# Optimization experiments

Measured on AMD Instinct MI355X. Metric: run time of the kernel, lower is better.

Reference implementation:

```python
import jax, jax.numpy as jnp
import numpy as np

INPUT_DIM = 1024
HIDDEN_DIM = 2048
NUM_EMB = 4096
EMB_DIM = 256
N = 65536


def setup_inputs() -> dict:
    key = jax.random.key(0)
    ks = jax.random.split(key, 10)
    s = lambda fan_in: 1.0 / np.sqrt(fan_in)
    return {
        "x": jax.random.normal(ks[0], (N, INPUT_DIM), dtype=jnp.float32),
        # encoder: Linear(input_dim, hidden) -> ReLU -> Linear(hidden, emb)
        "W1": jax.random.uniform(ks[1], (INPUT_DIM, HIDDEN_DIM), jnp.float32, -s(INPUT_DIM), s(INPUT_DIM)),
        "b1": jax.random.uniform(ks[2], (HIDDEN_DIM,), jnp.float32, -s(INPUT_DIM), s(INPUT_DIM)),
        "W2": jax.random.uniform(ks[3], (HIDDEN_DIM, EMB_DIM), jnp.float32, -s(HIDDEN_DIM), s(HIDDEN_DIM)),
        "b2": jax.random.uniform(ks[4], (EMB_DIM,), jnp.float32, -s(HIDDEN_DIM), s(HIDDEN_DIM)),
        # codebook (nn.Embedding weight)
        "codebook": jax.random.normal(ks[5], (NUM_EMB, EMB_DIM), dtype=jnp.float32),
        # decoder: Linear(emb, hidden) -> ReLU -> Linear(hidden, input_dim)
        "W3": jax.random.uniform(ks[6], (EMB_DIM, HIDDEN_DIM), jnp.float32, -s(EMB_DIM), s(EMB_DIM)),
        "b3": jax.random.uniform(ks[7], (HIDDEN_DIM,), jnp.float32, -s(EMB_DIM), s(EMB_DIM)),
        "W4": jax.random.uniform(ks[8], (HIDDEN_DIM, INPUT_DIM), jnp.float32, -s(HIDDEN_DIM), s(HIDDEN_DIM)),
        "b4": jax.random.uniform(ks[9], (INPUT_DIM,), jnp.float32, -s(HIDDEN_DIM), s(HIDDEN_DIM)),
    }


def reference(x, W1, b1, W2, b2, codebook, W3, b3, W4, b4):
    # encoder
    h = jax.nn.relu(x @ W1 + b1)
    encoded = h @ W2 + b2                      # [N, E]
    # cdist (squared form; argmin is identical to Euclidean argmin)
    enc_sq = jnp.sum(encoded * encoded, axis=-1, keepdims=True)   # [N, 1]
    cb_sq = jnp.sum(codebook * codebook, axis=-1)                 # [K]
    d2 = enc_sq - 2.0 * (encoded @ codebook.T) + cb_sq            # [N, K]
    indices = jnp.argmin(d2, axis=-1)                             # [N]
    quantized = codebook[indices]                                 # [N, E]
    # decoder
    h2 = jax.nn.relu(quantized @ W3 + b3)
    decoded = h2 @ W4 + b4
    return (quantized, decoded)
```

## Files before the change

kernel.cpp:

```cpp
#include <hip/hip_runtime.h>

#define N_ROWS 65536
#define IN_DIM 1024
#define HID    2048
#define EMB    256
#define NCODE  4096

typedef __attribute__((ext_vector_type(8))) short bf16x8;
typedef __attribute__((ext_vector_type(4))) float f32x4;

__device__ __forceinline__ unsigned short f2bf(float v) {
    unsigned u = __float_as_uint(v);
    u += 0x7FFFu + ((u >> 16) & 1u);
    return (unsigned short)(u >> 16);
}
__device__ __forceinline__ float bf2f(unsigned short h) {
    return __uint_as_float(((unsigned)h) << 16);
}
__device__ __forceinline__ void gload16(const unsigned short* g, unsigned short* l) {
    __builtin_amdgcn_global_load_lds(
        (const __attribute__((address_space(1))) unsigned int*)g,
        (__attribute__((address_space(3))) unsigned int*)l, 16, 0, 0);
}

template<int SPLIT>
__global__ __launch_bounds__(256) void k_conv_w(
    const float* __restrict__ src, unsigned short* __restrict__ dh,
    unsigned short* __restrict__ dl, int NC, int nkt)
{
    const int t = threadIdx.x;
    const int nt = blockIdx.x, kt = blockIdx.y;
    const int kk = t >> 2, j4 = (t & 3) << 2;
    const int k0 = kt << 6, n0 = nt << 4;
    float4 v = *(const float4*)(src + (size_t)(k0 + kk) * NC + n0 + j4);
    size_t tb = ((size_t)nt * nkt + kt) * 1024 + ((kk >> 3) * 128) + (kk & 7);
    float vv[4] = {v.x, v.y, v.z, v.w};
    #pragma unroll
    for (int j = 0; j < 4; ++j) {
        unsigned short h = f2bf(vv[j]);
        dh[tb + (size_t)(j4 + j) * 8] = h;
        if (SPLIT) dl[tb + (size_t)(j4 + j) * 8] = f2bf(vv[j] - bf2f(h));
    }
}

__global__ __launch_bounds__(256) void k_conv_a(
    const float* __restrict__ src, unsigned short* __restrict__ dst, int Kw, int nkt)
{
    const int t = threadIdx.x;
    const int mt = blockIdx.x, kt = blockIdx.y;
    const int rr = t >> 4, k4 = (t & 15) << 2;
    float4 v = *(const float4*)(src + (size_t)(mt * 16 + rr) * Kw + kt * 64 + k4);
    size_t addr = ((size_t)mt * nkt + kt) * 1024 + (k4 >> 3) * 128 + rr * 8 + (k4 & 7);
    ushort4 h = { f2bf(v.x), f2bf(v.y), f2bf(v.z), f2bf(v.w) };
    *(ushort4*)&dst[addr] = h;
}

__global__ __launch_bounds__(256) void k_conv_a2(
    const float* __restrict__ src, unsigned short* __restrict__ dh,
    unsigned short* __restrict__ dl, int Kw, int nkt)
{
    const int t = threadIdx.x;
    const int mt = blockIdx.x, kt = blockIdx.y;
    const int rr = t >> 4, k4 = (t & 15) << 2;
    float4 v = *(const float4*)(src + (size_t)(mt * 16 + rr) * Kw + kt * 64 + k4);
    size_t addr = ((size_t)mt * nkt + kt) * 1024 + (k4 >> 3) * 128 + rr * 8 + (k4 & 7);
    ushort4 h = { f2bf(v.x), f2bf(v.y), f2bf(v.z), f2bf(v.w) };
    ushort4 lo = { f2bf(v.x - bf2f(h.x)), f2bf(v.y - bf2f(h.y)),
                   f2bf(v.z - bf2f(h.z)), f2bf(v.w - bf2f(h.w)) };
    *(ushort4*)&dh[addr] = h;
    *(ushort4*)&dl[addr] = lo;
}

__global__ __launch_bounds__(256) void k_conv_cb(
    const float* __restrict__ cb, unsigned short* __restrict__ ch,
    unsigned short* __restrict__ cl_, float* __restrict__ halfsq)
{
    const int t = threadIdx.x;
    const int ct = blockIdx.x;
    const int cl = t >> 4, f = t & 15;
    const int code = (ct << 4) + cl;
    float ssq = 0.f;
    #pragma unroll
    for (int it = 0; it < 4; ++it) {
        const int k4 = (f << 2) + (it << 6);
        float4 v = *(const float4*)(cb + (size_t)code * EMB + k4);
        ssq += v.x * v.x + v.y * v.y + v.z * v.z + v.w * v.w;
        size_t tb = ((size_t)(ct * 4 + (k4 >> 6))) * 1024 + ((k4 >> 3) & 7) * 128 + cl * 8 + (k4 & 7);
        ushort4 h = { f2bf(v.x), f2bf(v.y), f2bf(v.z), f2bf(v.w) };
        *(ushort4*)&ch[tb] = h;
        ushort4 lo = { f2bf(v.x - bf2f(h.x)), f2bf(v.y - bf2f(h.y)),
                       f2bf(v.z - bf2f(h.z)), f2bf(v.w - bf2f(h.w)) };
        *(ushort4*)&cl_[tb] = lo;
    }
    #pragma unroll
    for (int off = 1; off <= 8; off <<= 1) ssq += __shfl_xor(ssq, off);
    if (f == 0) halfsq[code] = 0.5f * ssq;
}

template<int SPLIT, int AFMT, int OUTT>
__global__ __launch_bounds__(512, 1) void k_layer2(
    const float* __restrict__ A, const unsigned short* __restrict__ At,
    const unsigned short* __restrict__ Atl, int a_nkt,
    int lda, int K,
    const unsigned short* __restrict__ Bh, const unsigned short* __restrict__ Bl,
    int b_nkt, const float* __restrict__ bias, int biasoff,
    float* __restrict__ out, unsigned short* __restrict__ outt,
    unsigned short* __restrict__ outt2,
    int outw, int relu, int init, int ny_log2)
{
    constexpr int BUFSZ = SPLIT ? 32768 : 24576;
    constexpr int AL = 8192;
    constexpr int BH = SPLIT ? 16384 : 8192;
    __shared__ __align__(16) unsigned short s_mem[2 * BUFSZ];

    const int t = threadIdx.x;
    const int id = blockIdx.x;
    const int m_low = id & 7, rest = id >> 3;
    const int nb = rest & ((1 << ny_log2) - 1);
    const int m0 = (((rest >> ny_log2) << 3) | m_low) * 128;
    const int nb0 = nb * 256;
    const int lane = t & 63, wv = t >> 6;
    const int wm = wv >> 2, wn = wv & 3;
    const int g = lane >> 4, rr = lane & 15;
    const int nt = K >> 6;

    f32x4 acc[4][4];
    #pragma unroll
    for (int mi = 0; mi < 4; ++mi)
        #pragma unroll
        for (int ni = 0; ni < 4; ++ni) acc[mi][ni] = (f32x4){0.f, 0.f, 0.f, 0.f};

    #define STAGE_DMA(buf, ktile)                                                      \
        {                                                                              \
            unsigned short* base_ = &s_mem[(buf) * BUFSZ];                             \
            _Pragma("unroll")                                                          \
            for (int jj = 0; jj < 2; ++jj) {                                           \
                const int j_ = wv * 2 + jj;                                            \
                const size_t gt_ = ((size_t)(nb0 / 16 + j_) * b_nkt + (ktile)) * 1024; \
                _Pragma("unroll")                                                      \
                for (int hf = 0; hf < 2; ++hf)                                         \
                    gload16(Bh + gt_ + hf * 512 + lane * 8,                            \
                            base_ + BH + j_ * 1024 + hf * 512);                        \
            }                                                                          \
            if (AFMT >= 1) {                                                           \
                const size_t ga_ = ((size_t)(m0 / 16 + wv) * a_nkt + (ktile)) * 1024;  \
                _Pragma("unroll")                                                      \
                for (int hf = 0; hf < 2; ++hf)                                         \
                    gload16(At + ga_ + hf * 512 + lane * 8,                            \
                            base_ + wv * 1024 + hf * 512);                             \
                if (AFMT == 2) {                                                       \
                    _Pragma("unroll")                                                  \
                    for (int hf = 0; hf < 2; ++hf)                                     \
                        gload16(Atl + ga_ + hf * 512 + lane * 8,                       \
                                base_ + AL + wv * 1024 + hf * 512);                    \
                }                                                                      \
            }                                                                          \
        }

    #define A_LOAD(ktile, pv)                                                          \
        {                                                                              \
            _Pragma("unroll")                                                          \
            for (int it = 0; it < 4; ++it) {                                           \
                int f_ = t + (it << 9);                                                \
                int r_ = f_ >> 4, k4_ = (f_ & 15) << 2;                                \
                pv[it] = *(const float4*)(A + (size_t)(m0 + r_) * lda + (ktile) * 64 + k4_); \
            }                                                                          \
        }

    #define A_WRITE(buf, pv)                                                           \
        {                                                                              \
            unsigned short* base_ = &s_mem[(buf) * BUFSZ];                             \
            _Pragma("unroll")                                                          \
            for (int it = 0; it < 4; ++it) {                                           \
                int f_ = t + (it << 9);                                                \
                int r_ = f_ >> 4, k4_ = (f_ & 15) << 2;                                \
                int mt_ = r_ >> 4, rl_ = r_ & 15, kb_ = k4_ >> 3, e_ = k4_ & 7;        \
                int addr_ = mt_ * 1024 + kb_ * 128 + ((rl_ ^ kb_) << 3) + e_;          \
                float4 v_ = pv[it];                                                    \
                ushort4 hi_, lo_;                                                      \
                hi_.x = f2bf(v_.x); hi_.y = f2bf(v_.y); hi_.z = f2bf(v_.z); hi_.w = f2bf(v_.w); \
                *(ushort4*)&base_[addr_] = hi_;                                        \
                if (SPLIT) {                                                           \
                    lo_.x = f2bf(v_.x - bf2f(hi_.x)); lo_.y = f2bf(v_.y - bf2f(hi_.y)); \
                    lo_.z = f2bf(v_.z - bf2f(hi_.z)); lo_.w = f2bf(v_.w - bf2f(hi_.w)); \
                    *(ushort4*)&base_[AL + addr_] = lo_;                               \
                }                                                                      \
            }                                                                          \
        }

    #define COMPUTE(buf, ktile)                                                        \
        {                                                                              \
            const unsigned short* base_ = &s_mem[(buf) * BUFSZ];                       \
            __builtin_amdgcn_s_setprio(1);                                             \
            _Pragma("unroll")                                                          \
            for (int s = 0; s < 2; ++s) {                                              \
                const int kb = (s << 2) + g;                                           \
                bf16x8 a_h[4], a_l[4], b_h[4], b_l[4];                                 \
                _Pragma("unroll")                                                      \
                for (int i = 0; i < 4; ++i) {                                          \
                    int arow = (AFMT == 0) ? (((rr ^ kb) & 15) << 3) : (rr << 3);      \
                    int aaddr = (wm * 4 + i) * 1024 + kb * 128 + arow;                 \
                    a_h[i] = *(const bf16x8*)&base_[aaddr];                            \
                    if (SPLIT) a_l[i] = *(const bf16x8*)&base_[AL + aaddr];            \
                    int baddr = (wn * 4 + i) * 1024 + kb * 128 + (rr << 3);            \
                    b_h[i] = *(const bf16x8*)&base_[BH + baddr];                       \
                    if (SPLIT)                                                         \
                        b_l[i] = *(const bf16x8*)(Bl +                                 \
                            ((size_t)(nb0 / 16 + wn * 4 + i) * b_nkt + (ktile)) * 1024 \
                            + kb * 128 + (rr << 3));                                   \
                }                                                                      \
                _Pragma("unroll")                                                      \
                for (int mi = 0; mi < 4; ++mi)                                         \
                    _Pragma("unroll")                                                  \
                    for (int ni = 0; ni < 4; ++ni) {                                   \
                        acc[mi][ni] = __builtin_amdgcn_mfma_f32_16x16x32_bf16(a_h[mi], b_h[ni], acc[mi][ni], 0, 0, 0); \
                        if (SPLIT) {                                                   \
                            acc[mi][ni] = __builtin_amdgcn_mfma_f32_16x16x32_bf16(a_l[mi], b_h[ni], acc[mi][ni], 0, 0, 0); \
                            acc[mi][ni] = __builtin_amdgcn_mfma_f32_16x16x32_bf16(a_h[mi], b_l[ni], acc[mi][ni], 0, 0, 0); \
                        }                                                              \
                    }                                                                  \
            }                                                                          \
            __builtin_amdgcn_s_setprio(0);                                             \
        }

    float4 pv[4];
    STAGE_DMA(0, 0)
    if (AFMT == 0) {
        A_LOAD(0, pv)
        A_WRITE(0, pv)
    }
    asm volatile("s_waitcnt vmcnt(0) lgkmcnt(0)" ::: "memory");
    __builtin_amdgcn_s_barrier();
    __builtin_amdgcn_sched_barrier(0);

    int cur = 0;
    for (int kt = 0; kt < nt; ++kt) {
        if (kt + 1 < nt) {
            STAGE_DMA(cur ^ 1, kt + 1)
            if (AFMT == 0) A_LOAD(kt + 1, pv)
        }
        COMPUTE(cur, kt)
        if (AFMT == 0) { if (kt + 1 < nt) A_WRITE(cur ^ 1, pv) }
        asm volatile("s_waitcnt vmcnt(0) lgkmcnt(0)" ::: "memory");
        __builtin_amdgcn_s_barrier();
        __builtin_amdgcn_sched_barrier(0);
        cur ^= 1;
    }
    #undef STAGE_DMA
    #undef A_LOAD
    #undef A_WRITE
    #undef COMPUTE

    if (OUTT == 0) {
        float* sf = (float*)s_mem;
        for (int rm = 0; rm < 2; ++rm) {
            if (wm == rm) {
                #pragma unroll
                for (int mi = 0; mi < 4; ++mi)
                    #pragma unroll
                    for (int ni = 0; ni < 4; ++ni)
                        #pragma unroll
                        for (int rg = 0; rg < 4; ++rg)
                            sf[(mi * 16 + g * 4 + rg) * 256 + wn * 64 + ni * 16 + rr] = acc[mi][ni][rg];
            }
            __syncthreads();
            #pragma unroll
            for (int it = 0; it < 8; ++it) {
                int f = t + (it << 9);
                int r = f >> 6, c4 = (f & 63) << 2;
                float4 v = *(const float4*)&sf[r * 256 + c4];
                int gr = m0 + rm * 64 + r, gc = nb0 + c4;
                float* op = out + (size_t)gr * outw + gc;
                if (init) {
                    v.x += bias[biasoff + gc + 0]; v.y += bias[biasoff + gc + 1];
                    v.z += bias[biasoff + gc + 2]; v.w += bias[biasoff + gc + 3];
                } else {
                    float4 o = *(const float4*)op;
                    v.x += o.x; v.y += o.y; v.z += o.z; v.w += o.w;
                }
                if (relu) {
                    v.x = fmaxf(v.x, 0.f); v.y = fmaxf(v.y, 0.f);
                    v.z = fmaxf(v.z, 0.f); v.w = fmaxf(v.w, 0.f);
                }
                *(float4*)op = v;
            }
            __syncthreads();
        }
    } else {
        const int npass = (OUTT == 2) ? 2 : 1;
        for (int pass = 0; pass < npass; ++pass) {
            #pragma unroll
            for (int mi = 0; mi < 4; ++mi)
                #pragma unroll
                for (int ni = 0; ni < 4; ++ni) {
                    const int c = wn * 64 + ni * 16 + rr;
                    float bb = bias[biasoff + nb0 + c];
                    #pragma unroll
                    for (int rg = 0; rg < 4; ++rg) {
                        float v = acc[mi][ni][rg] + bb;
                        if (relu) v = fmaxf(v, 0.f);
                        unsigned short hi = f2bf(v);
                        unsigned short w = (pass == 0) ? hi : f2bf(v - bf2f(hi));
                        int addr = ((wm * 4 + mi) * 4 + wn) * 1024
                                 + (ni * 2 + (rr >> 3)) * 128 + (g * 4 + rg) * 8 + (rr & 7);
                        s_mem[addr] = w;
                    }
                }
            __syncthreads();
            unsigned short* dst = (pass == 0) ? outt : outt2;
            #pragma unroll
            for (int it = 0; it < 8; ++it) {
                int f = t + (it << 9);
                int tl = f >> 7, w8 = f & 127;
                size_t gaddr = ((size_t)(m0 / 16 + (tl >> 2)) * outw + nb0 / 64 + (tl & 3)) * 1024;
                *(float4*)(dst + gaddr + w8 * 8) = *(const float4*)&s_mem[tl * 1024 + w8 * 8];
            }
            __syncthreads();
        }
    }
}

__global__ __launch_bounds__(512, 2) void k_dist(
    float* encq, const unsigned short* __restrict__ ch,
    const unsigned short* __restrict__ cl,
    const float* __restrict__ hsq, const float* __restrict__ cb)
{
    __shared__ __align__(16) unsigned short s_cb[2][16384];
    __shared__ int s_c1[256], s_c2[256];

    const int t = threadIdx.x;
    const int lane = t & 63, wv = t >> 6;
    const int g = lane >> 4, rr = lane & 15;
    const int r0 = blockIdx.x * 256;

    bf16x8 eh[2][8], el[2][8];
    #pragma unroll
    for (int rg = 0; rg < 2; ++rg) {
        const float* ep = encq + (size_t)(r0 + wv * 32 + rg * 16 + rr) * EMB + g * 8;
        #pragma unroll
        for (int s = 0; s < 8; ++s) {
            float4 v0 = *(const float4*)(ep + s * 32);
            float4 v1 = *(const float4*)(ep + s * 32 + 4);
            float vv[8] = {v0.x, v0.y, v0.z, v0.w, v1.x, v1.y, v1.z, v1.w};
            bf16x8 a, b;
            #pragma unroll
            for (int j = 0; j < 8; ++j) {
                unsigned short h = f2bf(vv[j]);
                a[j] = (short)h;
                b[j] = (short)f2bf(vv[j] - bf2f(h));
            }
            eh[rg][s] = a; el[rg][s] = b;
        }
    }
    float b1v[2][4], b2v[2][4]; int i1v[2][4], i2v[2][4];
    #pragma unroll
    for (int rg = 0; rg < 2; ++rg)
        #pragma unroll
        for (int r2 = 0; r2 < 4; ++r2) {
            b1v[rg][r2] = -1e30f; b2v[rg][r2] = -1e30f;
            i1v[rg][r2] = 0; i2v[rg][r2] = 0;
        }

    #define STAGE(buf, c)                                                              \
        {                                                                              \
            const unsigned short* gh_ = ch + (size_t)(c) * 8192 + wv * 1024;           \
            const unsigned short* gl_ = cl + (size_t)(c) * 8192 + wv * 1024;           \
            _Pragma("unroll")                                                          \
            for (int i_ = 0; i_ < 2; ++i_) {                                           \
                gload16(gh_ + i_ * 512 + lane * 8, &s_cb[buf][wv * 1024 + i_ * 512]);  \
                gload16(gl_ + i_ * 512 + lane * 8, &s_cb[buf][8192 + wv * 1024 + i_ * 512]); \
            }                                                                          \
        }

    #define COMPUTE(cur, c, hv_)                                                       \
        {                                                                              \
            f32x4 ahh[2][2], ahl[2][2], alh[2][2];                                     \
            _Pragma("unroll")                                                          \
            for (int rg = 0; rg < 2; ++rg)                                             \
                _Pragma("unroll")                                                      \
                for (int ci = 0; ci < 2; ++ci) {                                       \
                    ahh[rg][ci] = (f32x4){0.f, 0.f, 0.f, 0.f};                         \
                    ahl[rg][ci] = (f32x4){0.f, 0.f, 0.f, 0.f};                         \
                    alh[rg][ci] = (f32x4){0.f, 0.f, 0.f, 0.f};                         \
                }                                                                      \
            __builtin_amdgcn_s_setprio(1);                                             \
            _Pragma("unroll")                                                          \
            for (int s = 0; s < 8; ++s) {                                              \
                const int ktile = s >> 1, kb = ((s & 1) << 2) + g;                     \
                _Pragma("unroll")                                                      \
                for (int ci = 0; ci < 2; ++ci) {                                       \
                    const int off = (ci * 4 + ktile) * 1024 + kb * 128 + rr * 8;       \
                    bf16x8 bh = *(const bf16x8*)&s_cb[cur][off];                       \
                    bf16x8 bl = *(const bf16x8*)&s_cb[cur][8192 + off];                \
                    _Pragma("unroll")                                                  \
                    for (int rg = 0; rg < 2; ++rg) {                                   \
                        ahh[rg][ci] = __builtin_amdgcn_mfma_f32_16x16x32_bf16(eh[rg][s], bh, ahh[rg][ci], 0, 0, 0); \
                        ahl[rg][ci] = __builtin_amdgcn_mfma_f32_16x16x32_bf16(eh[rg][s], bl, ahl[rg][ci], 0, 0, 0); \
                        alh[rg][ci] = __builtin_amdgcn_mfma_f32_16x16x32_bf16(el[rg][s], bh, alh[rg][ci], 0, 0, 0); \
                    }                                                                  \
                }                                                                      \
            }                                                                          \
            __builtin_amdgcn_s_setprio(0);                                             \
            _Pragma("unroll")                                                          \
            for (int rg = 0; rg < 2; ++rg)                                             \
                _Pragma("unroll")                                                      \
                for (int ci = 0; ci < 2; ++ci) {                                       \
                    f32x4 av = ahh[rg][ci] + ahl[rg][ci] + alh[rg][ci];                \
                    const int code = ((c) << 5) + (ci << 4) + rr;                      \
                    const float hs = __shfl(hv_, ci * 16 + rr);                        \
                    _Pragma("unroll")                                                  \
                    for (int r2 = 0; r2 < 4; ++r2) {                                   \
                        float v = av[r2] - hs;                                         \
                        bool bt1 = (v > b1v[rg][r2]) || (v == b1v[rg][r2] && code < i1v[rg][r2]); \
                        bool bt2 = (v > b2v[rg][r2]) || (v == b2v[rg][r2] && code < i2v[rg][r2]); \
                        if (bt1) { b2v[rg][r2] = b1v[rg][r2]; i2v[rg][r2] = i1v[rg][r2]; \
                                   b1v[rg][r2] = v; i1v[rg][r2] = code; }              \
                        else if (bt2) { b2v[rg][r2] = v; i2v[rg][r2] = code; }         \
                    }                                                                  \
                }                                                                      \
        }

    STAGE(0, 0)
    int cur = 0;
    for (int c = 0; c < 127; ++c) {
        STAGE(cur ^ 1, c + 1)
        float hv_ = hsq[(c << 5) + (lane & 31)];
        asm volatile("s_waitcnt vmcnt(5)" ::: "memory");
        __builtin_amdgcn_s_barrier();
        __builtin_amdgcn_sched_barrier(0);
        COMPUTE(cur, c, hv_)
        asm volatile("" ::: "memory");
        __builtin_amdgcn_s_barrier();
        cur ^= 1;
    }
    {
        float hv_ = hsq[(127 << 5) + (lane & 31)];
        asm volatile("s_waitcnt vmcnt(0)" ::: "memory");
        __builtin_amdgcn_s_barrier();
        __builtin_amdgcn_sched_barrier(0);
        COMPUTE(cur, 127, hv_)
    }
    #undef STAGE
    #undef COMPUTE

    #pragma unroll
    for (int off = 1; off <= 8; off <<= 1) {
        #pragma unroll
        for (int rg = 0; rg < 2; ++rg)
            #pragma unroll
            for (int r2 = 0; r2 < 4; ++r2) {
                float ob1 = __shfl_xor(b1v[rg][r2], off), ob2 = __shfl_xor(b2v[rg][r2], off);
                int oi1 = __shfl_xor(i1v[rg][r2], off), oi2 = __shfl_xor(i2v[rg][r2], off);
                bool ofirst = (ob1 > b1v[rg][r2]) || (ob1 == b1v[rg][r2] && oi1 < i1v[rg][r2]);
                if (ofirst) {
                    bool mysec = (b1v[rg][r2] > ob2) || (b1v[rg][r2] == ob2 && i1v[rg][r2] < oi2);
                    b2v[rg][r2] = mysec ? b1v[rg][r2] : ob2; i2v[rg][r2] = mysec ? i1v[rg][r2] : oi2;
                    b1v[rg][r2] = ob1; i1v[rg][r2] = oi1;
                } else {
                    bool osec = (ob1 > b2v[rg][r2]) || (ob1 == b2v[rg][r2] && oi1 < i2v[rg][r2]);
                    b2v[rg][r2] = osec ? ob1 : b2v[rg][r2]; i2v[rg][r2] = osec ? oi1 : i2v[rg][r2];
                }
            }
    }
    if (rr == 0) {
        #pragma unroll
        for (int rg = 0; rg < 2; ++rg)
            #pragma unroll
            for (int r2 = 0; r2 < 4; ++r2) {
                int rl = wv * 32 + rg * 16 + g * 4 + r2;
                s_c1[rl] = i1v[rg][r2]; s_c2[rl] = i2v[rg][r2];
            }
    }
    __syncthreads();

    for (int rloc = 0; rloc < 32; ++rloc) {
        const int row = wv * 32 + rloc;
        const int c1 = s_c1[row], c2 = s_c2[row];
        float4 ev = *(const float4*)(encq + (size_t)(r0 + row) * EMB + lane * 4);
        float4 v1 = *(const float4*)(cb + (size_t)c1 * EMB + lane * 4);
        float4 v2 = *(const float4*)(cb + (size_t)c2 * EMB + lane * 4);
        float d1 = ev.x * v1.x + ev.y * v1.y + ev.z * v1.z + ev.w * v1.w;
        float d2 = ev.x * v2.x + ev.y * v2.y + ev.z * v2.z + ev.w * v2.w;
        #pragma unroll
        for (int off = 1; off <= 32; off <<= 1) {
            d1 += __shfl_xor(d1, off);
            d2 += __shfl_xor(d2, off);
        }
        if (lane == 0) {
            float s1 = d1 - hsq[c1], s2 = d2 - hsq[c2];
            bool keep1 = (s1 > s2) || (s1 == s2 && c1 < c2);
            s_c1[row] = keep1 ? c1 : c2;
        }
    }
    __syncthreads();
    #pragma unroll
    for (int it = 0; it < 32; ++it) {
        int f = t + (it << 9);
        int row = f >> 6, c4 = (f & 63) << 2;
        int bi = s_c1[row];
        *(float4*)(encq + (size_t)(r0 + row) * EMB + c4) =
            *(const float4*)(cb + (size_t)bi * EMB + c4);
    }
}

__global__ __launch_bounds__(256) void k_dec_fb(
    const float* __restrict__ qz,
    const float* __restrict__ W3, const float* __restrict__ b3,
    const float* __restrict__ W4, const float* __restrict__ b4,
    float* __restrict__ outd) {
    __shared__ float s_q[8][EMB];
    __shared__ float s_h2[8][HID];
    const int t = threadIdx.x;
    const int row0 = blockIdx.x * 8;
    #pragma unroll
    for (int r = 0; r < 8; ++r) s_q[r][t] = qz[(size_t)(row0 + r) * EMB + t];
    __syncthreads();
    for (int gg = 0; gg < 8; ++gg) {
        const int j = (gg << 8) + t;
        float acc[8];
        #pragma unroll
        for (int r = 0; r < 8; ++r) acc[r] = 0.f;
        const float* wp = W3 + j;
        for (int e = 0; e < EMB; e += 4) {
            const float w0 = wp[(size_t)(e + 0) * HID];
            const float w1v = wp[(size_t)(e + 1) * HID];
            const float w2v = wp[(size_t)(e + 2) * HID];
            const float w3v = wp[(size_t)(e + 3) * HID];
            #pragma unroll
            for (int r = 0; r < 8; ++r) {
                const float4 qv = *reinterpret_cast<const float4*>(&s_q[r][e]);
                acc[r] = fmaf(qv.x, w0, acc[r]);
                acc[r] = fmaf(qv.y, w1v, acc[r]);
                acc[r] = fmaf(qv.z, w2v, acc[r]);
                acc[r] = fmaf(qv.w, w3v, acc[r]);
            }
        }
        const float bb = b3[j];
        #pragma unroll
        for (int r = 0; r < 8; ++r) s_h2[r][j] = fmaxf(acc[r] + bb, 0.f);
    }
    __syncthreads();
    float acc4[8][4];
    #pragma unroll
    for (int r = 0; r < 8; ++r)
        #pragma unroll
        for (int ci = 0; ci < 4; ++ci) acc4[r][ci] = 0.f;
    const float* w4p = W4 + t;
    for (int k = 0; k < HID; k += 4) {
        float wv[4][4];
        #pragma unroll
        for (int ki = 0; ki < 4; ++ki)
            #pragma unroll
            for (int ci = 0; ci < 4; ++ci)
                wv[ki][ci] = w4p[(size_t)(k + ki) * IN_DIM + (ci << 8)];
        #pragma unroll
        for (int r = 0; r < 8; ++r) {
            const float4 hv = *reinterpret_cast<const float4*>(&s_h2[r][k]);
            #pragma unroll
            for (int ci = 0; ci < 4; ++ci) {
                acc4[r][ci] = fmaf(hv.x, wv[0][ci], acc4[r][ci]);
                acc4[r][ci] = fmaf(hv.y, wv[1][ci], acc4[r][ci]);
                acc4[r][ci] = fmaf(hv.z, wv[2][ci], acc4[r][ci]);
                acc4[r][ci] = fmaf(hv.w, wv[3][ci], acc4[r][ci]);
            }
        }
    }
    #pragma unroll
    for (int ci = 0; ci < 4; ++ci) {
        const float bb = b4[(ci << 8) + t];
        #pragma unroll
        for (int r = 0; r < 8; ++r)
            outd[(size_t)(row0 + r) * IN_DIM + (ci << 8) + t] = acc4[r][ci] + bb;
    }
}

extern "C" void kernel_launch(void* const* d_in, const int* in_sizes, int n_in,
                              void* d_out, int out_size, void* d_ws, size_t ws_size,
                              hipStream_t stream) {
    const float* x  = (const float*)d_in[0];
    const float* W1 = (const float*)d_in[1];
    const float* b1 = (const float*)d_in[2];
    const float* W2 = (const float*)d_in[3];
    const float* b2 = (const float*)d_in[4];
    const float* cb = (const float*)d_in[5];
    const float* W3 = (const float*)d_in[6];
    const float* b3 = (const float*)d_in[7];
    const float* W4 = (const float*)d_in[8];
    const float* b4 = (const float*)d_in[9];

    float* outq = (float*)d_out;
    float* outd = outq + (size_t)N_ROWS * EMB;

    unsigned short* ou = (unsigned short*)outd;
    unsigned short* W1Th = ou;
    unsigned short* W1Tl = ou + 2097152;
    unsigned short* W2Th = ou + 4194304;
    unsigned short* W2Tl = ou + 4718592;
    unsigned short* cbh  = ou + 5242880;
    unsigned short* cbl  = ou + 6291456;
    float* halfsq = outd + 3670016;
    unsigned short* h_hi = (unsigned short*)(outd + 4194304);
    unsigned short* h_lo = h_hi + 33554432;
    unsigned short* qt = (unsigned short*)(outd + 58720256);
    float* enc = outq;

    const bool fastdec = ws_size >= (size_t)72351744;
    unsigned short* W3Th = (unsigned short*)d_ws;
    unsigned short* W4Th = W3Th + 524288;
    unsigned short* h2t  = (unsigned short*)((char*)d_ws + 5242880);
    unsigned short* xt_hi = h2t;
    unsigned short* xt_lo = h2t + 16777216;

    k_conv_w<1><<<dim3(128, 16), 256, 0, stream>>>(W1, W1Th, W1Tl, HID, 16);
    k_conv_w<1><<<dim3(16, 32), 256, 0, stream>>>(W2, W2Th, W2Tl, EMB, 32);
    k_conv_cb<<<256, 256, 0, stream>>>(cb, cbh, cbl, halfsq);
    if (fastdec) {
        k_conv_w<0><<<dim3(128, 4), 256, 0, stream>>>(W3, W3Th, nullptr, HID, 4);
        k_conv_w<0><<<dim3(64, 32), 256, 0, stream>>>(W4, W4Th, nullptr, IN_DIM, 32);
    }
    if (fastdec) {
        for (int s = 0; s < 4; ++s) {
            k_conv_a2<<<dim3(1024, 16), 256, 0, stream>>>(
                x + (size_t)s * 16777216, xt_hi, xt_lo, IN_DIM, 16);
            k_layer2<1, 2, 2><<<1024, 512, 0, stream>>>(
                nullptr, xt_hi, xt_lo, 16, 0, IN_DIM,
                W1Th, W1Tl, 16, b1, 0,
                nullptr, h_hi, h_lo, 32, 1, 0, 3);
            k_layer2<1, 2, 0><<<128, 512, 0, stream>>>(
                nullptr, h_hi, h_lo, 32, 0, HID,
                W2Th, W2Tl, 32, b2, 0,
                enc + (size_t)s * 4194304, nullptr, nullptr, EMB, 0, 1, 0);
        }
    } else {
        for (int q = 0; q < 4; ++q) {
            k_layer2<1, 0, 2><<<1024, 512, 0, stream>>>(
                x, nullptr, nullptr, 0, IN_DIM, IN_DIM,
                W1Th + (size_t)q * 524288, W1Tl + (size_t)q * 524288, 16,
                b1, q * 512, nullptr, h_hi, h_lo, 8, 1, 0, 1);
            k_layer2<1, 2, 0><<<512, 512, 0, stream>>>(
                nullptr, h_hi, h_lo, 8, 0, 512,
                W2Th + (size_t)q * 8192, W2Tl + (size_t)q * 8192, 32,
                b2, 0, enc, nullptr, nullptr, EMB, 0, q == 0, 0);
        }
    }
    k_dist<<<256, 512, 0, stream>>>(enc, cbh, cbl, halfsq, cb);
    if (fastdec) {
        k_conv_a<<<dim3(4096, 4), 256, 0, stream>>>(outq, qt, EMB, 4);
        for (int s = 0; s < 4; ++s) {
            const size_t roff = (size_t)s * 16384;
            k_layer2<0, 1, 1><<<1024, 512, 0, stream>>>(
                nullptr, qt + (size_t)s * 4194304, nullptr, 4, 0, EMB,
                W3Th, nullptr, 4,
                b3, 0, nullptr, h2t, nullptr, 32, 1, 0, 3);
            k_layer2<0, 1, 0><<<512, 512, 0, stream>>>(
                nullptr, h2t, nullptr, 32, 0, HID,
                W4Th, nullptr, 32,
                b4, 0, outd + roff * IN_DIM, nullptr, nullptr, IN_DIM, 0, 1, 2);
        }
    } else {
        k_dec_fb<<<N_ROWS / 8, 256, 0, stream>>>(outq, W3, b3, W4, b4, outd);
    }
}
```

Measured before the change: 2.359 ms.

## Restructure GEMM k-loop waits for DMA paths and fuse quantized bf16 conversion

For the DMA-fed A formats, the GEMM k-loop now issues the next stage's loads and waits only on the previous stage's outstanding loads with a partial vmcnt, then computes. A second barrier follows the compute, replacing the full vmcnt(0)/lgkmcnt(0) drain after compute, so prefetch overlaps compute. Separately, k_dist now writes the bf16 tiled copy of the quantized rows directly, removing the separate k_conv_a launch and its re-read of the quantized output. The hard-coded vmcnt counts depend on how many loads STAGE_DMA issues per format and could race if that count differs.

```diff
diff --git a/kernel.cpp b/kernel.cpp
--- a/kernel.cpp
+++ b/kernel.cpp
@@ -41,18 +41,6 @@
         dh[tb + (size_t)(j4 + j) * 8] = h;
         if (SPLIT) dl[tb + (size_t)(j4 + j) * 8] = f2bf(vv[j] - bf2f(h));
     }
-}
-
-__global__ __launch_bounds__(256) void k_conv_a(
-    const float* __restrict__ src, unsigned short* __restrict__ dst, int Kw, int nkt)
-{
-    const int t = threadIdx.x;
-    const int mt = blockIdx.x, kt = blockIdx.y;
-    const int rr = t >> 4, k4 = (t & 15) << 2;
-    float4 v = *(const float4*)(src + (size_t)(mt * 16 + rr) * Kw + kt * 64 + k4);
-    size_t addr = ((size_t)mt * nkt + kt) * 1024 + (k4 >> 3) * 128 + rr * 8 + (k4 & 7);
-    ushort4 h = { f2bf(v.x), f2bf(v.y), f2bf(v.z), f2bf(v.w) };
-    *(ushort4*)&dst[addr] = h;
 }
 
 __global__ __launch_bounds__(256) void k_conv_a2(
@@ -235,15 +223,30 @@
 
     int cur = 0;
     for (int kt = 0; kt < nt; ++kt) {
-        if (kt + 1 < nt) {
-            STAGE_DMA(cur ^ 1, kt + 1)
-            if (AFMT == 0) A_LOAD(kt + 1, pv)
-        }
-        COMPUTE(cur, kt)
-        if (AFMT == 0) { if (kt + 1 < nt) A_WRITE(cur ^ 1, pv) }
-        asm volatile("s_waitcnt vmcnt(0) lgkmcnt(0)" ::: "memory");
-        __builtin_amdgcn_s_barrier();
-        __builtin_amdgcn_sched_barrier(0);
+        if (AFMT >= 1) {
+            if (kt + 1 < nt) {
+                STAGE_DMA(cur ^ 1, kt + 1)
+                if (AFMT == 2) asm volatile("s_waitcnt vmcnt(8)" ::: "memory");
+                else           asm volatile("s_waitcnt vmcnt(6)" ::: "memory");
+            } else {
+                asm volatile("s_waitcnt vmcnt(0)" ::: "memory");
+            }
+            __builtin_amdgcn_s_barrier();
+            __builtin_amdgcn_sched_barrier(0);
+            COMPUTE(cur, kt)
+            asm volatile("" ::: "memory");
+            __builtin_amdgcn_s_barrier();
+        } else {
+            if (kt + 1 < nt) {
+                STAGE_DMA(cur ^ 1, kt + 1)
+                A_LOAD(kt + 1, pv)
+            }
+            COMPUTE(cur, kt)
+            if (kt + 1 < nt) A_WRITE(cur ^ 1, pv)
+            asm volatile("s_waitcnt vmcnt(0) lgkmcnt(0)" ::: "memory");
+            __builtin_amdgcn_s_barrier();
+            __builtin_amdgcn_sched_barrier(0);
+        }
         cur ^= 1;
     }
     #undef STAGE_DMA
@@ -323,7 +326,8 @@
 __global__ __launch_bounds__(512, 2) void k_dist(
     float* encq, const unsigned short* __restrict__ ch,
     const unsigned short* __restrict__ cl,
-    const float* __restrict__ hsq, const float* __restrict__ cb)
+    const float* __restrict__ hsq, const float* __restrict__ cb,
+    unsigned short* __restrict__ qt)
 {
     __shared__ __align__(16) unsigned short s_cb[2][16384];
     __shared__ int s_c1[256], s_c2[256];
@@ -498,8 +502,14 @@
         int f = t + (it << 9);
         int row = f >> 6, c4 = (f & 63) << 2;
         int bi = s_c1[row];
-        *(float4*)(encq + (size_t)(r0 + row) * EMB + c4) =
-            *(const float4*)(cb + (size_t)bi * EMB + c4);
+        float4 qv = *(const float4*)(cb + (size_t)bi * EMB + c4);
+        const int R = r0 + row;
+        *(float4*)(encq + (size_t)R * EMB + c4) = qv;
+        const int k4 = c4 & 63;
+        size_t qaddr = ((size_t)(R >> 4) * 4 + (c4 >> 6)) * 1024
+                     + (k4 >> 3) * 128 + (R & 15) * 8 + (k4 & 7);
+        ushort4 qh = { f2bf(qv.x), f2bf(qv.y), f2bf(qv.z), f2bf(qv.w) };
+        *(ushort4*)&qt[qaddr] = qh;
     }
 }
 
@@ -643,9 +653,8 @@
                 b2, 0, enc, nullptr, nullptr, EMB, 0, q == 0, 0);
         }
     }
-    k_dist<<<256, 512, 0, stream>>>(enc, cbh, cbl, halfsq, cb);
+    k_dist<<<256, 512, 0, stream>>>(enc, cbh, cbl, halfsq, cb, qt);
     if (fastdec) {
-        k_conv_a<<<dim3(4096, 4), 256, 0, stream>>>(outq, qt, EMB, 4);
         for (int s = 0; s < 4; ++s) {
             const size_t roff = (size_t)s * 16384;
             k_layer2<0, 1, 1><<<1024, 512, 0, stream>>>(
```

After: 2.426 ms. 1.03x slower.
